# Kernel tuning notes

Measured on AMD Instinct MI355X. Metric: run time of the kernel, lower is better.

The kernel has to match this reference:

```python
import jax, jax.numpy as jnp
import numpy as np

NUM_GENES = 20000
NUM_CLASS = 32
BATCH_SIZE = 8
N = NUM_GENES * BATCH_SIZE      # 160_000 total nodes
E = 2_560_000                    # edges (avg degree 16)
K = 10
ALPHA = 0.1


def setup_inputs() -> dict:
    key = jax.random.key(0)
    ks = jax.random.split(key, 9)
    x = jax.random.normal(ks[0], (N, 1), dtype=jnp.float32)
    edge_index = jax.random.randint(ks[1], (2, E), 0, N, dtype=jnp.int32)
    batch = jnp.repeat(jnp.arange(BATCH_SIZE, dtype=jnp.int32), NUM_GENES)
    exp_emb_table = jax.random.normal(ks[2], (NUM_GENES, NUM_CLASS), dtype=jnp.float32) * 0.1
    exp_bias_table = jax.random.normal(ks[3], (NUM_GENES, 1), dtype=jnp.float32) * 0.1
    s = 1.0 / np.sqrt(NUM_CLASS)
    W1 = jax.random.uniform(ks[4], (NUM_CLASS, NUM_CLASS), jnp.float32, -s, s)
    b1 = jax.random.uniform(ks[5], (NUM_CLASS,), jnp.float32, -s, s)
    W2 = jax.random.uniform(ks[6], (NUM_CLASS, NUM_CLASS), jnp.float32, -s, s)
    b2 = jax.random.uniform(ks[7], (NUM_CLASS,), jnp.float32, -s, s)
    return {"x": x, "edge_index": edge_index, "batch": batch,
            "exp_emb_table": exp_emb_table, "exp_bias_table": exp_bias_table,
            "W1": W1, "b1": b1, "W2": W2, "b2": b2}


def reference(x, edge_index, batch, exp_emb_table, exp_bias_table, W1, b1, W2, b2):
    # node_index tiles 0..num_genes-1 for each graph in the batch
    node_index = jnp.tile(jnp.arange(NUM_GENES), BATCH_SIZE)        # [N]
    h = exp_emb_table[node_index] * x + exp_bias_table[node_index]  # [N, C]
    # dropout is identity in eval mode
    h = jax.nn.relu(h @ W1.T + b1)
    h = h @ W2.T + b2

    # APPNP: gcn_norm with self-loops, then k power-iteration steps
    loops = jnp.arange(N, dtype=edge_index.dtype)
    row = jnp.concatenate([edge_index[0], loops])  # source
    col = jnp.concatenate([edge_index[1], loops])  # target
    deg = jax.ops.segment_sum(jnp.ones_like(col, dtype=h.dtype), col, num_segments=N)
    dinv = jnp.where(deg > 0, jax.lax.rsqrt(deg), 0.0)
    norm = (dinv[row] * dinv[col])[:, None]        # [E+N, 1]

    h0 = h
    def step(carry, _):
        agg = jax.ops.segment_sum(carry[row] * norm, col, num_segments=N)
        return (1.0 - ALPHA) * agg + ALPHA * h0, None
    h, _ = jax.lax.scan(step, h, None, length=K)

    # global mean pool over graphs
    sums = jax.ops.segment_sum(h, batch, num_segments=BATCH_SIZE)
    counts = jax.ops.segment_sum(jnp.ones((N, 1), h.dtype), batch, num_segments=BATCH_SIZE)
    return sums / counts  # [BATCH_SIZE, NUM_CLASS]
```

## Files before the change

kernel.cpp:

```cpp
#include <hip/hip_runtime.h>

typedef unsigned int u32;
typedef unsigned short u16;

#define NPB 64
#define CNTB 512
#define MSEG 16
#define PCHUNK 4096
#define SPB 16
#define DHCHUNK 8
#define OUT_CHUNK 640

__device__ inline float bf2f(u16 b) { return __uint_as_float(((u32)b) << 16); }
__device__ inline u16 f2bf(float f) {
    u32 u = __float_as_uint(f);
    return (u16)((u + 0x7fffu + ((u >> 16) & 1u)) >> 16);
}
__device__ inline u32 pack2(float a, float b) { return (u32)f2bf(a) | ((u32)f2bf(b) << 16); }

__global__ void k_zero_i(int* __restrict__ p, int n) {
    int i = blockIdx.x * 256 + threadIdx.x;
    if (i < n) p[i] = 0;
}

__global__ void k_cnt(const int* __restrict__ ei, int E,
                      int* __restrict__ pcnt, int nbuckets) {
    extern __shared__ int h[];
    int M = nbuckets + 64;
    for (int i = threadIdx.x; i < M; i += 256) h[i] = 0;
    __syncthreads();
    int stride = gridDim.x * 256;
    for (int e = blockIdx.x * 256 + threadIdx.x; e < E; e += stride) {
        atomicAdd(&h[ei[e] >> 6], 1);
        atomicAdd(&h[nbuckets + (ei[E + e] >> 12)], 1);
    }
    __syncthreads();
    int* dst = pcnt + (size_t)blockIdx.x * M;
    for (int i = threadIdx.x; i < M; i += 256) dst[i] = h[i];
}

__global__ void k_merge(const int* __restrict__ pcnt, int M, int nbuckets,
                        int* __restrict__ bcnt, int* __restrict__ dscnt) {
    int bin = blockIdx.x * 256 + threadIdx.x;
    if (bin >= M) return;
    const int per = CNTB / MSEG;
    const int* p = pcnt + (size_t)(blockIdx.y * per) * M + bin;
    int s0 = 0, s1 = 0, s2 = 0, s3 = 0;
    #pragma unroll
    for (int b = 0; b < per; b += 4) {
        s0 += p[(size_t)(b + 0) * M];
        s1 += p[(size_t)(b + 1) * M];
        s2 += p[(size_t)(b + 2) * M];
        s3 += p[(size_t)(b + 3) * M];
    }
    int s = s0 + s1 + s2 + s3;
    if (s) {
        if (bin < nbuckets) atomicAdd(&bcnt[bin], s);
        else atomicAdd(&dscnt[bin - nbuckets], s);
    }
}

__global__ void k_scanB(const int* __restrict__ bcnt, int nbuckets,
                        const int* __restrict__ dscnt,
                        int* __restrict__ boff, int* __restrict__ bCur,
                        int* __restrict__ soff, int* __restrict__ sCur,
                        int* __restrict__ dsoff, int* __restrict__ dsCur,
                        int* __restrict__ offsets, int N, int E, int nsup, int nsupD) {
    __shared__ int s[1024];
    __shared__ int carry;
    int t = threadIdx.x;
    if (t == 0) carry = 0;
    __syncthreads();
    for (int base = 0; base < nbuckets; base += 1024) {
        int i = base + t;
        int v = (i < nbuckets) ? bcnt[i] : 0;
        s[t] = v;
        __syncthreads();
        for (int off = 1; off < 1024; off <<= 1) {
            int tmp = (t >= off) ? s[t - off] : 0;
            __syncthreads();
            s[t] += tmp;
            __syncthreads();
        }
        int pos = s[t] - v + carry;
        if (i < nbuckets) {
            boff[i] = pos;
            bCur[i] = pos;
            if ((i & 63) == 0) { soff[i >> 6] = pos; sCur[i >> 6] = pos; }
        }
        __syncthreads();
        if (t == 1023) carry += s[1023];
        __syncthreads();
    }
    if (t == 0) {
        boff[nbuckets] = E; soff[nsup] = E; offsets[N] = E;
        int acc = 0;
        for (int i = 0; i < nsupD; ++i) {
            dsoff[i] = acc; dsCur[i] = acc;
            acc += dscnt[i];
        }
        dsoff[nsupD] = E;
    }
}

__global__ __launch_bounds__(512) void k_part(const int* __restrict__ ei, int E,
                                              int* __restrict__ sCur, int* __restrict__ dsCur,
                                              u32* __restrict__ buf1, u16* __restrict__ dbuf) {
    __shared__ int cnt[64];
    __shared__ int cur[64];
    __shared__ int dcnt[64];
    __shared__ int dcur[64];
    int c0 = blockIdx.x * PCHUNK;
    int c1 = min(E, c0 + PCHUNK);
    int t = threadIdx.x;
    if (t < 64) { cnt[t] = 0; dcnt[t] = 0; }
    __syncthreads();
    for (int e = c0 + t; e < c1; e += 512) {
        atomicAdd(&cnt[ei[e] >> 12], 1);
        atomicAdd(&dcnt[ei[E + e] >> 12], 1);
    }
    __syncthreads();
    if (t < 64) {
        int c = cnt[t];
        cur[t] = c ? atomicAdd(&sCur[t], c) : 0;
        int dc = dcnt[t];
        dcur[t] = dc ? atomicAdd(&dsCur[t], dc) : 0;
    }
    __syncthreads();
    for (int e = c0 + t; e < c1; e += 512) {
        int s = ei[e];
        int d = ei[E + e];
        int p = atomicAdd(&cur[s >> 12], 1);
        buf1[p] = (u32)(d & 0x3FFFF) | ((u32)(s & 4095) << 18);
        int pd = atomicAdd(&dcur[d >> 12], 1);
        dbuf[pd] = (u16)(d & 4095);
    }
}

__global__ __launch_bounds__(256) void k_dhist(const u16* __restrict__ dbuf,
                                               const int* __restrict__ dsoff,
                                               int* __restrict__ deg, int N) {
    __shared__ int h[4096];
    int sup = blockIdx.x / DHCHUNK;
    int ch = blockIdx.x % DHCHUNK;
    int t = threadIdx.x;
    for (int i = t; i < 4096; i += 256) h[i] = 0;
    __syncthreads();
    int s0 = dsoff[sup], s1 = dsoff[sup + 1];
    int per = (s1 - s0 + DHCHUNK - 1) / DHCHUNK;
    int c0 = s0 + ch * per;
    int c1 = min(s1, c0 + per);
    for (int e = c0 + t; e < c1; e += 256)
        atomicAdd(&h[dbuf[e]], 1);
    __syncthreads();
    int vbase = sup << 12;
    for (int i = t; i < 4096; i += 256) {
        int v = h[i];
        if (v && vbase + i < N) atomicAdd(&deg[vbase + i], v);
    }
}

__global__ __launch_bounds__(256) void k_p2(const u32* __restrict__ buf1,
                                            const int* __restrict__ soff,
                                            int* __restrict__ bCur,
                                            u32* __restrict__ binned) {
    __shared__ int cnt[64];
    __shared__ int cur[64];
    int sb = blockIdx.x / SPB;
    int ch = blockIdx.x % SPB;
    int s0 = soff[sb], s1 = soff[sb + 1];
    int per = (s1 - s0 + SPB - 1) / SPB;
    int c0 = s0 + ch * per;
    int c1 = min(s1, c0 + per);
    int t = threadIdx.x;
    if (t < 64) cnt[t] = 0;
    __syncthreads();
    for (int e = c0 + t; e < c1; e += 256)
        atomicAdd(&cnt[(buf1[e] >> 24) & 63], 1);
    __syncthreads();
    if (t < 64) {
        int c = cnt[t];
        cur[t] = (c > 0) ? atomicAdd(&bCur[(sb << 6) + t], c) : 0;
    }
    __syncthreads();
    for (int e = c0 + t; e < c1; e += 256) {
        u32 v = buf1[e];
        int p = atomicAdd(&cur[(v >> 24) & 63], 1);
        binned[p] = v & 0x00FFFFFFu;
    }
}

__global__ __launch_bounds__(256) void k_sort(const u32* __restrict__ binned,
                                              const int* __restrict__ boff,
                                              int* __restrict__ offsets,
                                              int* __restrict__ dsts, int N) {
    __shared__ int cnt[64];
    __shared__ int off[64];
    int b = blockIdx.x;
    int s0 = boff[b], s1 = boff[b + 1];
    int t = threadIdx.x;
    if (t < 64) cnt[t] = 0;
    __syncthreads();
    for (int e = s0 + t; e < s1; e += 256)
        atomicAdd(&cnt[(binned[e] >> 18) & 63], 1);
    __syncthreads();
    if (t == 0) {
        int acc = s0;
        #pragma unroll
        for (int i = 0; i < 64; ++i) { off[i] = acc; acc += cnt[i]; }
    }
    __syncthreads();
    int vbase = b << 6;
    if (t < 64 && vbase + t < N) offsets[vbase + t] = off[t];
    __syncthreads();
    if (t < 64) cnt[t] = off[t];
    __syncthreads();
    for (int e = s0 + t; e < s1; e += 256) {
        u32 v = binned[e];
        int p = atomicAdd(&cnt[(v >> 18) & 63], 1);
        dsts[p] = (int)(v & 0x3FFFFu);
    }
}

__global__ void k_dinv(const int* __restrict__ deg, float* __restrict__ dinv,
                       float* __restrict__ a, float* __restrict__ rd, int N) {
    int i = blockIdx.x * 256 + threadIdx.x;
    if (i < N) {
        float d = (float)(deg[i] + 1);
        float dv = rsqrtf(d);
        dinv[i] = dv;
        a[i] = 0.9f * dv * dv;
        rd[i] = sqrtf(d);
    }
}

__global__ __launch_bounds__(256) void k_AW(const float* __restrict__ emb,
                                            const float* __restrict__ W1,
                                            float* __restrict__ A, int ngenes) {
    __shared__ float w1[32][33];
    __shared__ float eb[8][33];
    int t = threadIdx.x;
    int j = t & 31, gl = t >> 5;
    for (int i = t; i < 1024; i += 256) w1[i >> 5][i & 31] = W1[i];
    int g = blockIdx.x * 8 + gl;
    if (g < ngenes) eb[gl][j] = emb[g * 32 + j];
    __syncthreads();
    if (g < ngenes) {
        float acc = 0.f;
        #pragma unroll
        for (int c = 0; c < 32; ++c) acc = fmaf(eb[gl][c], w1[j][c], acc);
        A[(size_t)g * 32 + j] = acc;
    }
}

__global__ void k_s1(const float* __restrict__ W1, float* __restrict__ s1) {
    int j = threadIdx.x;
    if (j < 32) {
        float acc = 0.f;
        #pragma unroll
        for (int c = 0; c < 32; ++c) acc += W1[j * 32 + c];
        s1[j] = acc;
    }
}

__global__ __launch_bounds__(256) void k_h0(const float* __restrict__ x,
                                            const float* __restrict__ A,
                                            const float* __restrict__ bias,
                                            const float* __restrict__ s1,
                                            const float* __restrict__ b1,
                                            const float* __restrict__ W2,
                                            const float* __restrict__ b2,
                                            const float* __restrict__ dinv,
                                            uint4* __restrict__ h0,
                                            uint4* __restrict__ q0,
                                            float* __restrict__ out, int out_n,
                                            int N, int ngenes) {
    int node = blockIdx.x * 256 + threadIdx.x;
    if (blockIdx.x == 0 && threadIdx.x < out_n) out[threadIdx.x] = 0.f;
    if (node >= N) return;
    int g = node % ngenes;
    float xv = x[node];
    float bv = bias[g];
    const float4* Ar = (const float4*)(A + (size_t)g * 32);
    float r1[32];
    #pragma unroll
    for (int q = 0; q < 8; ++q) {
        float4 a4 = Ar[q];
        r1[q * 4 + 0] = fmaxf(fmaf(xv, a4.x, fmaf(bv, s1[q * 4 + 0], b1[q * 4 + 0])), 0.f);
        r1[q * 4 + 1] = fmaxf(fmaf(xv, a4.y, fmaf(bv, s1[q * 4 + 1], b1[q * 4 + 1])), 0.f);
        r1[q * 4 + 2] = fmaxf(fmaf(xv, a4.z, fmaf(bv, s1[q * 4 + 2], b1[q * 4 + 2])), 0.f);
        r1[q * 4 + 3] = fmaxf(fmaf(xv, a4.w, fmaf(bv, s1[q * 4 + 3], b1[q * 4 + 3])), 0.f);
    }
    u32 ow[16];
    #pragma unroll
    for (int i = 0; i < 32; i += 2) {
        float accA = b2[i];
        float accB = b2[i + 1];
        #pragma unroll
        for (int j2 = 0; j2 < 32; ++j2) {
            accA = fmaf(r1[j2], W2[i * 32 + j2], accA);
            accB = fmaf(r1[j2], W2[(i + 1) * 32 + j2], accB);
        }
        ow[i >> 1] = pack2(accA * 1.0f, accB * 1.0f);
    }
    #pragma unroll
    for (int q = 0; q < 4; ++q) {
        uint4 o;
        o.x = ow[q * 4 + 0];
        o.y = ow[q * 4 + 1];
        o.z = ow[q * 4 + 2];
        o.w = ow[q * 4 + 3];
        h0[(size_t)node * 4 + q] = o;
    }
    int gb = node / ngenes;
    u32 lo = (u32)f2bf(dinv[node]);
    u32 hi = lo << 16;
    uint4 qo;
    qo.x = (gb == 0) ? lo : (gb == 1) ? hi : 0u;
    qo.y = (gb == 2) ? lo : (gb == 3) ? hi : 0u;
    qo.z = (gb == 4) ? lo : (gb == 5) ? hi : 0u;
    qo.w = (gb == 6) ? lo : (gb == 7) ? hi : 0u;
    q0[node] = qo;
}

__global__ __launch_bounds__(256) void k_prop8(const uint4* __restrict__ qin,
                                               uint4* __restrict__ qout,
                                               const float* __restrict__ a,
                                               const float* __restrict__ dinv,
                                               const int* __restrict__ offsets,
                                               const int* __restrict__ dsts,
                                               int N, int ngenes) {
    int node = blockIdx.x * 256 + threadIdx.x;
    if (node >= N) return;
    int s0 = offsets[node];
    int s1 = offsets[node + 1];
    uint4 self = qin[node];
    float c0 = bf2f((u16)self.x), c1 = bf2f((u16)(self.x >> 16));
    float c2 = bf2f((u16)self.y), c3 = bf2f((u16)(self.y >> 16));
    float c4 = bf2f((u16)self.z), c5 = bf2f((u16)(self.z >> 16));
    float c6 = bf2f((u16)self.w), c7 = bf2f((u16)(self.w >> 16));
    int e = s0;
    for (; e + 4 <= s1; e += 4) {
        uint4 vA = qin[dsts[e]];
        uint4 vB = qin[dsts[e + 1]];
        uint4 vC = qin[dsts[e + 2]];
        uint4 vD = qin[dsts[e + 3]];
        c0 += bf2f((u16)vA.x) + bf2f((u16)vB.x) + bf2f((u16)vC.x) + bf2f((u16)vD.x);
        c1 += bf2f((u16)(vA.x >> 16)) + bf2f((u16)(vB.x >> 16)) + bf2f((u16)(vC.x >> 16)) + bf2f((u16)(vD.x >> 16));
        c2 += bf2f((u16)vA.y) + bf2f((u16)vB.y) + bf2f((u16)vC.y) + bf2f((u16)vD.y);
        c3 += bf2f((u16)(vA.y >> 16)) + bf2f((u16)(vB.y >> 16)) + bf2f((u16)(vC.y >> 16)) + bf2f((u16)(vD.y >> 16));
        c4 += bf2f((u16)vA.z) + bf2f((u16)vB.z) + bf2f((u16)vC.z) + bf2f((u16)vD.z);
        c5 += bf2f((u16)(vA.z >> 16)) + bf2f((u16)(vB.z >> 16)) + bf2f((u16)(vC.z >> 16)) + bf2f((u16)(vD.z >> 16));
        c6 += bf2f((u16)vA.w) + bf2f((u16)vB.w) + bf2f((u16)vC.w) + bf2f((u16)vD.w);
        c7 += bf2f((u16)(vA.w >> 16)) + bf2f((u16)(vB.w >> 16)) + bf2f((u16)(vC.w >> 16)) + bf2f((u16)(vD.w >> 16));
    }
    for (; e < s1; ++e) {
        uint4 v = qin[dsts[e]];
        c0 += bf2f((u16)v.x); c1 += bf2f((u16)(v.x >> 16));
        c2 += bf2f((u16)v.y); c3 += bf2f((u16)(v.y >> 16));
        c4 += bf2f((u16)v.z); c5 += bf2f((u16)(v.z >> 16));
        c6 += bf2f((u16)v.w); c7 += bf2f((u16)(v.w >> 16));
    }
    float av = a[node];
    float qi = 0.1f * dinv[node];
    int gb = node / ngenes;
    c0 = av * c0 + ((gb == 0) ? qi : 0.f);
    c1 = av * c1 + ((gb == 1) ? qi : 0.f);
    c2 = av * c2 + ((gb == 2) ? qi : 0.f);
    c3 = av * c3 + ((gb == 3) ? qi : 0.f);
    c4 = av * c4 + ((gb == 4) ? qi : 0.f);
    c5 = av * c5 + ((gb == 5) ? qi : 0.f);
    c6 = av * c6 + ((gb == 6) ? qi : 0.f);
    c7 = av * c7 + ((gb == 7) ? qi : 0.f);
    uint4 o;
    o.x = pack2(c0, c1);
    o.y = pack2(c2, c3);
    o.z = pack2(c4, c5);
    o.w = pack2(c6, c7);
    qout[node] = o;
}

__global__ __launch_bounds__(256) void k_out(const uint4* __restrict__ q,
                                             const u16* __restrict__ h0,
                                             const float* __restrict__ rd,
                                             float* __restrict__ out,
                                             int N, int ngenes) {
    __shared__ float wq[64][8];
    __shared__ u16 hs[64][32];
    int t = threadIdx.x;
    int b = t >> 5, c = t & 31;
    float acc = 0.f;
    int base = blockIdx.x * OUT_CHUNK;
    int lim = min(N, base + OUT_CHUNK);
    for (int v0 = base; v0 < lim; v0 += 64) {
        int nv = min(64, lim - v0);
        __syncthreads();
        int r = t >> 2, w4 = t & 3;
        if (r < nv) {
            *(uint4*)&hs[r][w4 * 8] = ((const uint4*)(h0 + (size_t)(v0 + r) * 32))[w4];
            u32 wv = ((const u32*)&q[v0 + r])[w4];
            float rdv = rd[v0 + r];
            wq[r][w4 * 2] = bf2f((u16)wv) * rdv;
            wq[r][w4 * 2 + 1] = bf2f((u16)(wv >> 16)) * rdv;
        }
        __syncthreads();
        for (int i = 0; i < nv; ++i)
            acc = fmaf(wq[i][b], bf2f(hs[i][c]), acc);
    }
    atomicAdd(&out[b * 32 + c], acc / (float)ngenes);
}

extern "C" void kernel_launch(void* const* d_in, const int* in_sizes, int n_in,
                              void* d_out, int out_size, void* d_ws, size_t ws_size,
                              hipStream_t stream) {
    const float* x    = (const float*)d_in[0];
    const int*   ei   = (const int*)d_in[1];
    const float* emb  = (const float*)d_in[3];
    const float* bias = (const float*)d_in[4];
    const float* W1   = (const float*)d_in[5];
    const float* b1   = (const float*)d_in[6];
    const float* W2   = (const float*)d_in[7];
    const float* b2   = (const float*)d_in[8];
    float* out = (float*)d_out;

    int N = in_sizes[0];
    int E = in_sizes[1] / 2;
    int ngenes = in_sizes[4];
    int nbuckets = (N + NPB - 1) / NPB;
    int nsup = (nbuckets + 63) / 64;
    int nsupD = (N + 4095) / 4096;
    int M = nbuckets + 64;

    char* pws = (char*)d_ws;
    auto carve = [&](size_t bytes) {
        void* r = (void*)pws;
        pws += (bytes + 255) & ~(size_t)255;
        return r;
    };
    u16*   h0      = (u16*)carve((size_t)N * 32 * 2);
    uint4* qA      = (uint4*)carve((size_t)N * 16);
    uint4* qB      = (uint4*)carve((size_t)N * 16);
    float* Amat    = (float*)carve((size_t)ngenes * 32 * 4);
    float* s1v     = (float*)carve(32 * 4);
    float* dinv    = (float*)carve((size_t)N * 4);
    float* afac    = (float*)carve((size_t)N * 4);
    float* rd      = (float*)carve((size_t)N * 4);
    int*   offsets = (int*)carve((size_t)(N + 1) * 4);
    int*   deg     = (int*)carve((size_t)N * 4);
    int*   bcnt    = (int*)carve((size_t)nbuckets * 4);
    int*   dscnt   = (int*)carve(64 * 4);
    int*   boff    = (int*)carve((size_t)(nbuckets + 1) * 4);
    int*   bCur    = (int*)carve((size_t)nbuckets * 4);
    int*   soff    = (int*)carve(65 * 4);
    int*   sCur    = (int*)carve(64 * 4);
    int*   dsoff   = (int*)carve(65 * 4);
    int*   dsCur   = (int*)carve(64 * 4);
    int*   pcnt    = (int*)carve((size_t)CNTB * M * 4);
    u32*   buf1    = (u32*)carve((size_t)E * 4);
    u32*   binned  = (u32*)carve((size_t)E * 4);
    int*   dsts    = (int*)carve((size_t)E * 4);
    u16*   dbuf    = (u16*)carve((size_t)E * 2);

    int nbN = (N + 255) / 256;
    int zlen = (int)(dscnt - deg) + 64;

    hipLaunchKernelGGL(k_zero_i, dim3((zlen + 255) / 256), dim3(256), 0, stream, deg, zlen);
    hipLaunchKernelGGL(k_cnt, dim3(CNTB), dim3(256), M * 4, stream, ei, E, pcnt, nbuckets);
    hipLaunchKernelGGL(k_merge, dim3((M + 255) / 256, MSEG), dim3(256), 0, stream,
                       pcnt, M, nbuckets, bcnt, dscnt);
    hipLaunchKernelGGL(k_scanB, dim3(1), dim3(1024), 0, stream,
                       bcnt, nbuckets, dscnt, boff, bCur, soff, sCur, dsoff, dsCur,
                       offsets, N, E, nsup, nsupD);
    hipLaunchKernelGGL(k_part, dim3((E + PCHUNK - 1) / PCHUNK), dim3(512), 0, stream,
                       ei, E, sCur, dsCur, buf1, dbuf);
    hipLaunchKernelGGL(k_dhist, dim3(nsupD * DHCHUNK), dim3(256), 0, stream,
                       dbuf, dsoff, deg, N);
    hipLaunchKernelGGL(k_dinv, dim3(nbN), dim3(256), 0, stream, deg, dinv, afac, rd, N);
    hipLaunchKernelGGL(k_p2, dim3(nsup * SPB), dim3(256), 0, stream, buf1, soff, bCur, binned);
    hipLaunchKernelGGL(k_sort, dim3(nbuckets), dim3(256), 0, stream,
                       binned, boff, offsets, dsts, N);
    hipLaunchKernelGGL(k_AW, dim3((ngenes + 7) / 8), dim3(256), 0, stream, emb, W1, Amat, ngenes);
    hipLaunchKernelGGL(k_s1, dim3(1), dim3(64), 0, stream, W1, s1v);
    hipLaunchKernelGGL(k_h0, dim3(nbN), dim3(256), 0, stream,
                       x, Amat, bias, s1v, b1, W2, b2, dinv,
                       (uint4*)h0, qA, out, out_size, N, ngenes);

    const uint4* qin = qA;
    for (int it = 0; it < 10; ++it) {
        uint4* qo = (it & 1) ? qA : qB;
        hipLaunchKernelGGL(k_prop8, dim3(nbN), dim3(256), 0, stream,
                           qin, qo, afac, dinv, offsets, dsts, N, ngenes);
        qin = qo;
    }

    hipLaunchKernelGGL(k_out, dim3((N + OUT_CHUNK - 1) / OUT_CHUNK), dim3(256), 0, stream,
                       qin, h0, rd, out, N, ngenes);
}
```

Measured before the change: 367.0 us.

## Fuse ten propagation launches into one cooperative kernel with grid sync

Replaces the ten separate k_prop8 launches with a single cooperative kernel. It loops over the propagation steps, ping-pongs between the two buffers and calls grid.sync between steps. Per-node constants (offsets, scale factor, teleport term) are now loaded once and kept in registers across iterations. This removes repeated kernel-launch gaps and redundant loads, but relies on all 625 blocks being co-resident and adds a grid-wide barrier cost per step.

```diff
diff --git a/kernel.cpp b/kernel.cpp
--- a/kernel.cpp
+++ b/kernel.cpp
@@ -1,4 +1,7 @@
 #include <hip/hip_runtime.h>
+#include <hip/hip_cooperative_groups.h>
+
+namespace cg = cooperative_groups;
 
 typedef unsigned int u32;
 typedef unsigned short u16;
@@ -301,7 +304,7 @@
             accA = fmaf(r1[j2], W2[i * 32 + j2], accA);
             accB = fmaf(r1[j2], W2[(i + 1) * 32 + j2], accB);
         }
-        ow[i >> 1] = pack2(accA * 1.0f, accB * 1.0f);
+        ow[i >> 1] = pack2(accA, accB);
     }
     #pragma unroll
     for (int q = 0; q < 4; ++q) {
@@ -323,61 +326,76 @@
     q0[node] = qo;
 }
 
-__global__ __launch_bounds__(256) void k_prop8(const uint4* __restrict__ qin,
-                                               uint4* __restrict__ qout,
+__global__ __launch_bounds__(256) void k_propN(uint4* __restrict__ qAb,
+                                               uint4* __restrict__ qBb,
                                                const float* __restrict__ a,
                                                const float* __restrict__ dinv,
                                                const int* __restrict__ offsets,
                                                const int* __restrict__ dsts,
-                                               int N, int ngenes) {
+                                               int N, int ngenes, int steps) {
+    cg::grid_group grid = cg::this_grid();
     int node = blockIdx.x * 256 + threadIdx.x;
-    if (node >= N) return;
-    int s0 = offsets[node];
-    int s1 = offsets[node + 1];
-    uint4 self = qin[node];
-    float c0 = bf2f((u16)self.x), c1 = bf2f((u16)(self.x >> 16));
-    float c2 = bf2f((u16)self.y), c3 = bf2f((u16)(self.y >> 16));
-    float c4 = bf2f((u16)self.z), c5 = bf2f((u16)(self.z >> 16));
-    float c6 = bf2f((u16)self.w), c7 = bf2f((u16)(self.w >> 16));
-    int e = s0;
-    for (; e + 4 <= s1; e += 4) {
-        uint4 vA = qin[dsts[e]];
-        uint4 vB = qin[dsts[e + 1]];
-        uint4 vC = qin[dsts[e + 2]];
-        uint4 vD = qin[dsts[e + 3]];
-        c0 += bf2f((u16)vA.x) + bf2f((u16)vB.x) + bf2f((u16)vC.x) + bf2f((u16)vD.x);
-        c1 += bf2f((u16)(vA.x >> 16)) + bf2f((u16)(vB.x >> 16)) + bf2f((u16)(vC.x >> 16)) + bf2f((u16)(vD.x >> 16));
-        c2 += bf2f((u16)vA.y) + bf2f((u16)vB.y) + bf2f((u16)vC.y) + bf2f((u16)vD.y);
-        c3 += bf2f((u16)(vA.y >> 16)) + bf2f((u16)(vB.y >> 16)) + bf2f((u16)(vC.y >> 16)) + bf2f((u16)(vD.y >> 16));
-        c4 += bf2f((u16)vA.z) + bf2f((u16)vB.z) + bf2f((u16)vC.z) + bf2f((u16)vD.z);
-        c5 += bf2f((u16)(vA.z >> 16)) + bf2f((u16)(vB.z >> 16)) + bf2f((u16)(vC.z >> 16)) + bf2f((u16)(vD.z >> 16));
-        c6 += bf2f((u16)vA.w) + bf2f((u16)vB.w) + bf2f((u16)vC.w) + bf2f((u16)vD.w);
-        c7 += bf2f((u16)(vA.w >> 16)) + bf2f((u16)(vB.w >> 16)) + bf2f((u16)(vC.w >> 16)) + bf2f((u16)(vD.w >> 16));
-    }
-    for (; e < s1; ++e) {
-        uint4 v = qin[dsts[e]];
-        c0 += bf2f((u16)v.x); c1 += bf2f((u16)(v.x >> 16));
-        c2 += bf2f((u16)v.y); c3 += bf2f((u16)(v.y >> 16));
-        c4 += bf2f((u16)v.z); c5 += bf2f((u16)(v.z >> 16));
-        c6 += bf2f((u16)v.w); c7 += bf2f((u16)(v.w >> 16));
-    }
-    float av = a[node];
-    float qi = 0.1f * dinv[node];
-    int gb = node / ngenes;
-    c0 = av * c0 + ((gb == 0) ? qi : 0.f);
-    c1 = av * c1 + ((gb == 1) ? qi : 0.f);
-    c2 = av * c2 + ((gb == 2) ? qi : 0.f);
-    c3 = av * c3 + ((gb == 3) ? qi : 0.f);
-    c4 = av * c4 + ((gb == 4) ? qi : 0.f);
-    c5 = av * c5 + ((gb == 5) ? qi : 0.f);
-    c6 = av * c6 + ((gb == 6) ? qi : 0.f);
-    c7 = av * c7 + ((gb == 7) ? qi : 0.f);
-    uint4 o;
-    o.x = pack2(c0, c1);
-    o.y = pack2(c2, c3);
-    o.z = pack2(c4, c5);
-    o.w = pack2(c6, c7);
-    qout[node] = o;
+    bool active = node < N;
+    int s0 = 0, s1 = 0;
+    float av = 0.f, i0 = 0.f, i1 = 0.f, i2 = 0.f, i3 = 0.f, i4 = 0.f, i5 = 0.f, i6 = 0.f, i7 = 0.f;
+    if (active) {
+        s0 = offsets[node];
+        s1 = offsets[node + 1];
+        av = a[node];
+        float qi = 0.1f * dinv[node];
+        int gb = node / ngenes;
+        i0 = (gb == 0) ? qi : 0.f;
+        i1 = (gb == 1) ? qi : 0.f;
+        i2 = (gb == 2) ? qi : 0.f;
+        i3 = (gb == 3) ? qi : 0.f;
+        i4 = (gb == 4) ? qi : 0.f;
+        i5 = (gb == 5) ? qi : 0.f;
+        i6 = (gb == 6) ? qi : 0.f;
+        i7 = (gb == 7) ? qi : 0.f;
+    }
+    const uint4* qin = qAb;
+    uint4* qout = qBb;
+    for (int it = 0; it < steps; ++it) {
+        if (active) {
+            uint4 self = qin[node];
+            float c0 = bf2f((u16)self.x), c1 = bf2f((u16)(self.x >> 16));
+            float c2 = bf2f((u16)self.y), c3 = bf2f((u16)(self.y >> 16));
+            float c4 = bf2f((u16)self.z), c5 = bf2f((u16)(self.z >> 16));
+            float c6 = bf2f((u16)self.w), c7 = bf2f((u16)(self.w >> 16));
+            int e = s0;
+            for (; e + 4 <= s1; e += 4) {
+                uint4 vA = qin[dsts[e]];
+                uint4 vB = qin[dsts[e + 1]];
+                uint4 vC = qin[dsts[e + 2]];
+                uint4 vD = qin[dsts[e + 3]];
+                c0 += bf2f((u16)vA.x) + bf2f((u16)vB.x) + bf2f((u16)vC.x) + bf2f((u16)vD.x);
+                c1 += bf2f((u16)(vA.x >> 16)) + bf2f((u16)(vB.x >> 16)) + bf2f((u16)(vC.x >> 16)) + bf2f((u16)(vD.x >> 16));
+                c2 += bf2f((u16)vA.y) + bf2f((u16)vB.y) + bf2f((u16)vC.y) + bf2f((u16)vD.y);
+                c3 += bf2f((u16)(vA.y >> 16)) + bf2f((u16)(vB.y >> 16)) + bf2f((u16)(vC.y >> 16)) + bf2f((u16)(vD.y >> 16));
+                c4 += bf2f((u16)vA.z) + bf2f((u16)vB.z) + bf2f((u16)vC.z) + bf2f((u16)vD.z);
+                c5 += bf2f((u16)(vA.z >> 16)) + bf2f((u16)(vB.z >> 16)) + bf2f((u16)(vC.z >> 16)) + bf2f((u16)(vD.z >> 16));
+                c6 += bf2f((u16)vA.w) + bf2f((u16)vB.w) + bf2f((u16)vC.w) + bf2f((u16)vD.w);
+                c7 += bf2f((u16)(vA.w >> 16)) + bf2f((u16)(vB.w >> 16)) + bf2f((u16)(vC.w >> 16)) + bf2f((u16)(vD.w >> 16));
+            }
+            for (; e < s1; ++e) {
+                uint4 v = qin[dsts[e]];
+                c0 += bf2f((u16)v.x); c1 += bf2f((u16)(v.x >> 16));
+                c2 += bf2f((u16)v.y); c3 += bf2f((u16)(v.y >> 16));
+                c4 += bf2f((u16)v.z); c5 += bf2f((u16)(v.z >> 16));
+                c6 += bf2f((u16)v.w); c7 += bf2f((u16)(v.w >> 16));
+            }
+            uint4 o;
+            o.x = pack2(fmaf(av, c0, i0), fmaf(av, c1, i1));
+            o.y = pack2(fmaf(av, c2, i2), fmaf(av, c3, i3));
+            o.z = pack2(fmaf(av, c4, i4), fmaf(av, c5, i5));
+            o.w = pack2(fmaf(av, c6, i6), fmaf(av, c7, i7));
+            qout[node] = o;
+        }
+        grid.sync();
+        const uint4* tmp = qout;
+        qout = (uint4*)qin;
+        qin = tmp;
+    }
 }
 
 __global__ __launch_bounds__(256) void k_out(const uint4* __restrict__ q,
@@ -485,14 +503,11 @@
                        x, Amat, bias, s1v, b1, W2, b2, dinv,
                        (uint4*)h0, qA, out, out_size, N, ngenes);
 
-    const uint4* qin = qA;
-    for (int it = 0; it < 10; ++it) {
-        uint4* qo = (it & 1) ? qA : qB;
-        hipLaunchKernelGGL(k_prop8, dim3(nbN), dim3(256), 0, stream,
-                           qin, qo, afac, dinv, offsets, dsts, N, ngenes);
-        qin = qo;
-    }
+    int steps = 10;
+    void* args[] = { (void*)&qA, (void*)&qB, (void*)&afac, (void*)&dinv,
+                     (void*)&offsets, (void*)&dsts, (void*)&N, (void*)&ngenes, (void*)&steps };
+    hipLaunchCooperativeKernel((const void*)k_propN, dim3(nbN), dim3(256), args, 0, stream);
 
     hipLaunchKernelGGL(k_out, dim3((N + OUT_CHUNK - 1) / OUT_CHUNK), dim3(256), 0, stream,
-                       qin, h0, rd, out, N, ngenes);
-}
+                       qA, h0, rd, out, N, ngenes);
+}
```

Result: slower. 1.202 ms (+227.4%).
